# Optimization experiments

Measured on AMD Instinct MI355X. Metric: run time of the kernel, lower is better.

## Reference

```python
import jax, jax.numpy as jnp
import numpy as np

B, NELEC, NATOMS, SH_PER_ATOM, NORB, NCTR = 512, 100, 20, 30, 300, 2
NBAS = NATOMS * SH_PER_ATOM  # 600 == NORB * NCTR


def _ipow(x, k):
    # x**k for integer k in {0,1,2}; safe for negative x (cartesian harmonics)
    return jnp.where(k == 0, jnp.ones_like(x), jnp.where(k == 1, x, x * x))


def setup_inputs() -> dict:
    key = jax.random.key(0)
    ks = jax.random.split(key, 7)
    pos = jax.random.normal(ks[0], (B, NELEC * 3), jnp.float32)
    atom_coords = jax.random.normal(ks[1], (NATOMS, 3), jnp.float32)
    bas_exp = jax.random.uniform(ks[2], (NBAS,), jnp.float32, 0.5, 3.0)
    bas_n = jax.random.randint(ks[3], (NBAS,), 0, 3).astype(jnp.float32)
    norm_cst = jax.random.uniform(ks[4], (NBAS,), jnp.float32, 0.5, 1.5)
    bas_coeffs = jax.random.normal(ks[5], (NBAS,), jnp.float32)
    bas_kxyz = jax.random.randint(ks[6], (NBAS, 3), 0, 3)  # kx, ky, kz exponents
    index_ctr = jnp.repeat(jnp.arange(NORB, dtype=jnp.int32), NCTR)  # nbas -> norb
    return {"pos": pos, "atom_coords": atom_coords, "bas_exp": bas_exp,
            "bas_n": bas_n, "norm_cst": norm_cst, "bas_coeffs": bas_coeffs,
            "bas_kxyz": bas_kxyz, "index_ctr": index_ctr}


def reference(pos, atom_coords, bas_exp, bas_n, norm_cst, bas_coeffs, bas_kxyz, index_ctr):
    # gather: per-shell atom coordinates  (NBAS, 3)
    bas_coords = jnp.repeat(atom_coords, SH_PER_ATOM, axis=0)
    # electron - basis-center displacement  (B, Nelec, NBAS, 3)
    xyz = pos.reshape(-1, NELEC, 1, 3) - bas_coords[None, None]
    r2 = jnp.sum(xyz * xyz, axis=-1)                 # (B, Nelec, NBAS)
    r = jnp.sqrt(r2)
    # radial_gaussian: r^n * exp(-alpha r^2)
    R = jnp.power(r, bas_n) * jnp.exp(-bas_exp * r2)
    # cartesian harmonics: x^kx * y^ky * z^kz
    Y = (_ipow(xyz[..., 0], bas_kxyz[:, 0]) *
         _ipow(xyz[..., 1], bas_kxyz[:, 1]) *
         _ipow(xyz[..., 2], bas_kxyz[:, 2]))
    # ao kernel + contraction (segment-sum over basis fns into orbitals)
    vals = (norm_cst * bas_coeffs) * R * Y           # (B, Nelec, NBAS)
    ao = jnp.zeros((pos.shape[0], NELEC, NORB), vals.dtype).at[:, :, index_ctr].add(vals)
    return ao
```

## Files before the change

### kernel.cpp

```cpp
#include <hip/hip_runtime.h>

#define BATCH   512
#define NELEC   100
#define NATOMS  20
#define SH      30
#define NORB    300
#define NBAS    600
#define NROWS   (BATCH * NELEC)
#define GROWS   32
#define NBLOCKS (NROWS / GROWS)
#define BLOCK   320

#define LOG2E 1.4426950408889634f

__global__ __launch_bounds__(BLOCK, 8) void ao_kernel(
    const float* __restrict__ pos,
    const float* __restrict__ atom_coords,
    const float* __restrict__ bas_exp,
    const float* __restrict__ bas_n,
    const float* __restrict__ norm_cst,
    const float* __restrict__ bas_coeffs,
    const int*   __restrict__ bas_kxyz,
    float*       __restrict__ out)
{
    __shared__ float4 spos4[GROWS];

    const int t    = threadIdx.x;
    const int row0 = blockIdx.x * GROWS;

    float2 ex2, nn2, nc2, bc2;
    int2 k01, k23, k45;
    float ax = 0.f, ay = 0.f, az = 0.f;
    if (t < NORB) {
        ex2 = ((const float2*)bas_exp)[t];
        nn2 = ((const float2*)bas_n)[t];
        nc2 = ((const float2*)norm_cst)[t];
        bc2 = ((const float2*)bas_coeffs)[t];
        k01 = ((const int2*)bas_kxyz)[3 * t + 0];
        k23 = ((const int2*)bas_kxyz)[3 * t + 1];
        k45 = ((const int2*)bas_kxyz)[3 * t + 2];
        const int at = (2 * t) / SH;
        ax = atom_coords[3 * at + 0];
        ay = atom_coords[3 * at + 1];
        az = atom_coords[3 * at + 2];
    }

    if (t < GROWS * 3) {
        ((float*)spos4)[(t / 3) * 4 + (t % 3)] = pos[(size_t)row0 * 3 + t];
    }
    __syncthreads();

    if (t < NORB) {
        const float c0 = nc2.x * bc2.x;
        const float c1 = nc2.y * bc2.y;
        const float al0 = -ex2.x * LOG2E;
        const float al1 = -ex2.y * LOG2E;
        const int n0 = (int)nn2.x, n1 = (int)nn2.y;
        const float q00 = (n0 == 0) ? c0 : 0.0f, q01 = (n0 == 1) ? c0 : 0.0f, q02 = (n0 == 2) ? c0 : 0.0f;
        const float q10 = (n1 == 0) ? c1 : 0.0f, q11 = (n1 == 1) ? c1 : 0.0f, q12 = (n1 == 2) ? c1 : 0.0f;
        const int kx0 = k01.x, ky0 = k01.y, kz0 = k23.x;
        const int kx1 = k23.y, ky1 = k45.x, kz1 = k45.y;
        const float mx00 = (kx0 == 0), mx01 = (kx0 == 1), mx02 = (kx0 == 2);
        const float my00 = (ky0 == 0), my01 = (ky0 == 1), my02 = (ky0 == 2);
        const float mz00 = (kz0 == 0), mz01 = (kz0 == 1), mz02 = (kz0 == 2);
        const float mx10 = (kx1 == 0), mx11 = (kx1 == 1), mx12 = (kx1 == 2);
        const float my10 = (ky1 == 0), my11 = (ky1 == 1), my12 = (ky1 == 2);
        const float mz10 = (kz1 == 0), mz11 = (kz1 == 1), mz12 = (kz1 == 2);

        float* op = out + (size_t)row0 * NORB + t;

#pragma unroll 4
        for (int r = 0; r < GROWS; ++r) {
            const float4 p = spos4[r];

            const float dx = p.x - ax, dy = p.y - ay, dz = p.z - az;
            const float r2 = fmaf(dx, dx, fmaf(dy, dy, dz * dz));
            const float rr = __builtin_amdgcn_sqrtf(r2);

            float e  = __builtin_amdgcn_exp2f(al0 * r2);
            float cR = fmaf(rr, q01, fmaf(r2, q02, q00));
            float yx = fmaf(dx, fmaf(dx, mx02, mx01), mx00);
            float yy = fmaf(dy, fmaf(dy, my02, my01), my00);
            float yz = fmaf(dz, fmaf(dz, mz02, mz01), mz00);
            float v  = (cR * e) * ((yx * yy) * yz);

            e  = __builtin_amdgcn_exp2f(al1 * r2);
            cR = fmaf(rr, q11, fmaf(r2, q12, q10));
            yx = fmaf(dx, fmaf(dx, mx12, mx11), mx10);
            yy = fmaf(dy, fmaf(dy, my12, my11), my10);
            yz = fmaf(dz, fmaf(dz, mz12, mz11), mz10);
            v  = fmaf(cR * e, (yx * yy) * yz, v);

            *op = v;
            op += NORB;
        }
    }
}

extern "C" void kernel_launch(void* const* d_in, const int* in_sizes, int n_in,
                              void* d_out, int out_size, void* d_ws, size_t ws_size,
                              hipStream_t stream) {
    const float* pos         = (const float*)d_in[0];
    const float* atom_coords = (const float*)d_in[1];
    const float* bas_exp     = (const float*)d_in[2];
    const float* bas_n       = (const float*)d_in[3];
    const float* norm_cst    = (const float*)d_in[4];
    const float* bas_coeffs  = (const float*)d_in[5];
    const int*   bas_kxyz    = (const int*)d_in[6];
    float* out = (float*)d_out;

    ao_kernel<<<NBLOCKS, BLOCK, 0, stream>>>(pos, atom_coords, bas_exp, bas_n,
                                             norm_cst, bas_coeffs, bas_kxyz, out);
}
```

Baseline: 102.1 us.

## Map lanes to rows and waves to atoms, stage outputs in LDS for float4 stores

Threads now map to electron rows (lanes) while each wave handles one atom's 15 orbitals. The displacement, r2 and sqrt are computed once per lane and reused across all orbitals of that atom, and the per-orbital parameters are wave-uniform scalar loads. Results go into a padded LDS tile and are written back as coalesced float4 stores. This removes the idle threads left by the 300-of-320 mapping and the repeated per-orbital distance work. In exchange it adds an LDS round trip, a barrier, and scalar parameter loads inside the loop.

```diff
diff --git a/kernel.cpp b/kernel.cpp
--- a/kernel.cpp
+++ b/kernel.cpp
@@ -7,9 +7,16 @@
 #define NORB    300
 #define NBAS    600
 #define NROWS   (BATCH * NELEC)
-#define GROWS   32
-#define NBLOCKS (NROWS / GROWS)
-#define BLOCK   320
+#define RPB     64
+#define OPW     15
+#define WPB     4
+#define OPB     (OPW * WPB)
+#define NOBLK   (NORB / OPB)
+#define NRBLK   (NROWS / RPB)
+#define NBLOCKS (NOBLK * NRBLK)
+#define BLOCK   (64 * WPB)
+#define LSTR    65
+#define NQ      (OPB / 4)
 
 #define LOG2E 1.4426950408889634f
 
@@ -23,41 +30,48 @@
     const int*   __restrict__ bas_kxyz,
     float*       __restrict__ out)
 {
-    __shared__ float4 spos4[GROWS];
+    __shared__ float sres[RPB * LSTR];
 
     const int t    = threadIdx.x;
-    const int row0 = blockIdx.x * GROWS;
+    const int lane = t & 63;
+    const int wave = t >> 6;
+    const int ob   = blockIdx.x % NOBLK;
+    const int rb   = blockIdx.x / NOBLK;
+    const int row  = rb * RPB + lane;
 
-    float2 ex2, nn2, nc2, bc2;
-    int2 k01, k23, k45;
-    float ax = 0.f, ay = 0.f, az = 0.f;
-    if (t < NORB) {
-        ex2 = ((const float2*)bas_exp)[t];
-        nn2 = ((const float2*)bas_n)[t];
-        nc2 = ((const float2*)norm_cst)[t];
-        bc2 = ((const float2*)bas_coeffs)[t];
-        k01 = ((const int2*)bas_kxyz)[3 * t + 0];
-        k23 = ((const int2*)bas_kxyz)[3 * t + 1];
-        k45 = ((const int2*)bas_kxyz)[3 * t + 2];
-        const int at = (2 * t) / SH;
-        ax = atom_coords[3 * at + 0];
-        ay = atom_coords[3 * at + 1];
-        az = atom_coords[3 * at + 2];
-    }
+    const float px = pos[row * 3 + 0];
+    const float py = pos[row * 3 + 1];
+    const float pz = pos[row * 3 + 2];
 
-    if (t < GROWS * 3) {
-        ((float*)spos4)[(t / 3) * 4 + (t % 3)] = pos[(size_t)row0 * 3 + t];
-    }
-    __syncthreads();
+    const int atom = __builtin_amdgcn_readfirstlane(ob * WPB + wave);
+    const float ax = atom_coords[atom * 3 + 0];
+    const float ay = atom_coords[atom * 3 + 1];
+    const float az = atom_coords[atom * 3 + 2];
 
-    if (t < NORB) {
+    const float dx = px - ax, dy = py - ay, dz = pz - az;
+    const float r2 = fmaf(dx, dx, fmaf(dy, dy, dz * dz));
+    const float rr = __builtin_amdgcn_sqrtf(r2);
+
+    const int o0 = atom * OPW;
+
+#pragma unroll 5
+    for (int oi = 0; oi < OPW; ++oi) {
+        const int og = __builtin_amdgcn_readfirstlane(o0 + oi);
+        const float2 ex2 = ((const float2*)bas_exp)[og];
+        const float2 nn2 = ((const float2*)bas_n)[og];
+        const float2 nc2 = ((const float2*)norm_cst)[og];
+        const float2 bc2 = ((const float2*)bas_coeffs)[og];
+        const int2 k01 = ((const int2*)bas_kxyz)[3 * og + 0];
+        const int2 k23 = ((const int2*)bas_kxyz)[3 * og + 1];
+        const int2 k45 = ((const int2*)bas_kxyz)[3 * og + 2];
+
         const float c0 = nc2.x * bc2.x;
         const float c1 = nc2.y * bc2.y;
         const float al0 = -ex2.x * LOG2E;
         const float al1 = -ex2.y * LOG2E;
         const int n0 = (int)nn2.x, n1 = (int)nn2.y;
-        const float q00 = (n0 == 0) ? c0 : 0.0f, q01 = (n0 == 1) ? c0 : 0.0f, q02 = (n0 == 2) ? c0 : 0.0f;
-        const float q10 = (n1 == 0) ? c1 : 0.0f, q11 = (n1 == 1) ? c1 : 0.0f, q12 = (n1 == 2) ? c1 : 0.0f;
+        const float q00 = (n0 == 0) ? c0 : 0.f, q01 = (n0 == 1) ? c0 : 0.f, q02 = (n0 == 2) ? c0 : 0.f;
+        const float q10 = (n1 == 0) ? c1 : 0.f, q11 = (n1 == 1) ? c1 : 0.f, q12 = (n1 == 2) ? c1 : 0.f;
         const int kx0 = k01.x, ky0 = k01.y, kz0 = k23.x;
         const int kx1 = k23.y, ky1 = k45.x, kz1 = k45.y;
         const float mx00 = (kx0 == 0), mx01 = (kx0 == 1), mx02 = (kx0 == 2);
@@ -67,33 +81,31 @@
         const float my10 = (ky1 == 0), my11 = (ky1 == 1), my12 = (ky1 == 2);
         const float mz10 = (kz1 == 0), mz11 = (kz1 == 1), mz12 = (kz1 == 2);
 
-        float* op = out + (size_t)row0 * NORB + t;
+        float e  = __builtin_amdgcn_exp2f(al0 * r2);
+        float cR = fmaf(rr, q01, fmaf(r2, q02, q00));
+        float yx = fmaf(dx, fmaf(dx, mx02, mx01), mx00);
+        float yy = fmaf(dy, fmaf(dy, my02, my01), my00);
+        float yz = fmaf(dz, fmaf(dz, mz02, mz01), mz00);
+        float v  = (cR * e) * ((yx * yy) * yz);
 
-#pragma unroll 4
-        for (int r = 0; r < GROWS; ++r) {
-            const float4 p = spos4[r];
+        e  = __builtin_amdgcn_exp2f(al1 * r2);
+        cR = fmaf(rr, q11, fmaf(r2, q12, q10));
+        yx = fmaf(dx, fmaf(dx, mx12, mx11), mx10);
+        yy = fmaf(dy, fmaf(dy, my12, my11), my10);
+        yz = fmaf(dz, fmaf(dz, mz12, mz11), mz10);
+        v  = fmaf(cR * e, (yx * yy) * yz, v);
 
-            const float dx = p.x - ax, dy = p.y - ay, dz = p.z - az;
-            const float r2 = fmaf(dx, dx, fmaf(dy, dy, dz * dz));
-            const float rr = __builtin_amdgcn_sqrtf(r2);
+        sres[lane * LSTR + (wave * OPW + oi)] = v;
+    }
+    __syncthreads();
 
-            float e  = __builtin_amdgcn_exp2f(al0 * r2);
-            float cR = fmaf(rr, q01, fmaf(r2, q02, q00));
-            float yx = fmaf(dx, fmaf(dx, mx02, mx01), mx00);
-            float yy = fmaf(dy, fmaf(dy, my02, my01), my00);
-            float yz = fmaf(dz, fmaf(dz, mz02, mz01), mz00);
-            float v  = (cR * e) * ((yx * yy) * yz);
-
-            e  = __builtin_amdgcn_exp2f(al1 * r2);
-            cR = fmaf(rr, q11, fmaf(r2, q12, q10));
-            yx = fmaf(dx, fmaf(dx, mx12, mx11), mx10);
-            yy = fmaf(dy, fmaf(dy, my12, my11), my10);
-            yz = fmaf(dz, fmaf(dz, mz12, mz11), mz10);
-            v  = fmaf(cR * e, (yx * yy) * yz, v);
-
-            *op = v;
-            op += NORB;
-        }
+    float* obase = out + (size_t)rb * RPB * NORB + ob * OPB;
+    for (int i = t; i < RPB * NQ; i += BLOCK) {
+        const int r = i / NQ, q = i - r * NQ;
+        const float* s = &sres[r * LSTR + q * 4];
+        float4 v;
+        v.x = s[0]; v.y = s[1]; v.z = s[2]; v.w = s[3];
+        *(float4*)(obase + (size_t)r * NORB + q * 4) = v;
     }
 }
 
```

New measurement: 111.2 us. 9.0% more time.
